# Kernel optimization log

Hardware: AMD Instinct MI355X
Metric: run time of the kernel (lower is better)

## Reference

```python
import jax, jax.numpy as jnp
import numpy as np
import math

D_MODEL = 1024
D_STATE = 16
D_CONV = 4
EXPAND = 2
D_INNER = EXPAND * D_MODEL
DT_RANK = max(D_MODEL // 16, 1)
B_SZ, L_SEQ = 2, 2048
DT_MIN, DT_MAX = 1e-3, 1e-1


def setup_inputs() -> dict:
    key = jax.random.key(0)
    ks = jax.random.split(key, 10)
    x = jax.random.normal(ks[0], (B_SZ, L_SEQ, D_MODEL), dtype=jnp.float32)
    # torch nn.Linear weights are [out, in]
    in_proj_w = jax.random.normal(ks[1], (2 * D_INNER, D_MODEL), jnp.float32) * 0.02
    conv_w = jax.random.normal(ks[2], (D_INNER, 1, D_CONV), jnp.float32) * 0.2  # depthwise [d,1,k]
    conv_b = jax.random.normal(ks[3], (D_INNER,), jnp.float32) * 0.02
    x_proj_w = jax.random.normal(ks[4], (DT_RANK + 2 * D_STATE, D_INNER), jnp.float32) * 0.02
    dt_init_std = DT_RANK ** -0.5
    dt_proj_w = jax.random.uniform(ks[5], (D_INNER, DT_RANK), jnp.float32, -dt_init_std, dt_init_std)
    dt = jnp.exp(jax.random.uniform(ks[6], (D_INNER,)) * (math.log(DT_MAX) - math.log(DT_MIN)) + math.log(DT_MIN))
    dt = jnp.clip(dt, DT_MIN, None)
    dt_proj_b = dt + jnp.log(-jnp.expm1(-dt))  # inverse softplus
    A = jnp.tile(jnp.arange(1, D_STATE + 1, dtype=jnp.float32)[None, :], (D_INNER, 1))
    A_log = jnp.log(A)
    D_param = jnp.ones((D_INNER,), jnp.float32)
    out_proj_w = jax.random.normal(ks[7], (D_MODEL, D_INNER), jnp.float32) * 0.02
    return {"x": x, "in_proj_w": in_proj_w, "conv_w": conv_w, "conv_b": conv_b,
            "x_proj_w": x_proj_w, "dt_proj_w": dt_proj_w, "dt_proj_b": dt_proj_b,
            "A_log": A_log, "D_param": D_param, "out_proj_w": out_proj_w}


def _ssm_forward(x, in_proj_w, conv_w, conv_b, x_proj_w, dt_proj_w, dt_proj_b, A_log, D_param, out_proj_w):
    B, L, _ = x.shape
    xz = jnp.einsum('bld,ed->ble', x, in_proj_w)          # [B,L,2*d_inner]
    x_branch, z = jnp.split(xz, 2, axis=-1)               # each [B,L,d_inner]
    # causal depthwise conv over L
    xc = jnp.transpose(x_branch, (0, 2, 1))               # [B,d,L]
    xc = jnp.pad(xc, ((0, 0), (0, 0), (D_CONV - 1, 0)))
    xc = jax.lax.conv_general_dilated(xc, conv_w, window_strides=(1,), padding='VALID',
                                      feature_group_count=D_INNER)
    xc = xc + conv_b[None, :, None]
    x_conv = jax.nn.silu(jnp.transpose(xc, (0, 2, 1)))    # [B,L,d_inner]
    # input-dependent projections
    xp = jnp.einsum('bld,ed->ble', x_conv, x_proj_w)      # [B,L,dt_rank+2n]
    dt_low, Bp, Cp = jnp.split(xp, [DT_RANK, DT_RANK + D_STATE], axis=-1)
    dt = jax.nn.softplus(jnp.einsum('blr,dr->bld', dt_low, dt_proj_w) + dt_proj_b)  # [B,L,d]
    A = -jnp.exp(A_log)                                   # [d,n]
    # sequential selective scan via lax.scan (time-major inputs)
    def step(h, inp):
        dt_t, B_t, C_t, x_t = inp                         # [B,d],[B,n],[B,n],[B,d]
        dA = jnp.exp(dt_t[:, :, None] * A[None])          # [B,d,n]
        h = dA * h + (dt_t * x_t)[:, :, None] * B_t[:, None, :]
        y = jnp.einsum('bdn,bn->bd', h, C_t)
        return h, y

    h0 = jnp.zeros((B, D_INNER, D_STATE), x.dtype)
    xs = (jnp.swapaxes(dt, 0, 1), jnp.swapaxes(Bp, 0, 1), jnp.swapaxes(Cp, 0, 1), jnp.swapaxes(x_conv, 0, 1))
    _, ys = jax.lax.scan(step, h0, xs)                    # ys: [L,B,d]
    y = jnp.swapaxes(ys, 0, 1)                            # [B,L,d]
    y = y + D_param * x_conv
    y = y * jax.nn.silu(z)
    return jnp.einsum('bld,ed->ble', y, out_proj_w)       # [B,L,d_model]


def reference(x, in_proj_w, conv_w, conv_b, x_proj_w, dt_proj_w, dt_proj_b, A_log, D_param, out_proj_w):
    return _ssm_forward(x, in_proj_w, conv_w, conv_b, x_proj_w, dt_proj_w, dt_proj_b, A_log, D_param, out_proj_w)
```

## Files before the change

### kernel.cpp

```cpp
#include <hip/hip_runtime.h>
#include <math.h>

#define BB      2
#define LSEQ    2048
#define DMODEL  1024
#define DINNER  2048
#define DSTATE  16
#define DTRANK  64
#define NPROJ   96
#define MROWS   (BB * LSEQ)
#define NCHUNK  64
#define CLEN    32
#define XKS     16

typedef short bf16x8 __attribute__((ext_vector_type(8)));
typedef float f32x4  __attribute__((ext_vector_type(4)));

struct HL { unsigned int hx, hy, lx, ly; };

__device__ __forceinline__ HL cvt4(float4 v) {
  unsigned int ux = __float_as_uint(v.x), uy = __float_as_uint(v.y);
  unsigned int uz = __float_as_uint(v.z), uw = __float_as_uint(v.w);
  unsigned int tx = ux & 0xFFFF0000u, ty = uy & 0xFFFF0000u;
  unsigned int tz = uz & 0xFFFF0000u, tw = uw & 0xFFFF0000u;
  HL r;
  r.hx = (tx >> 16) | ty;
  r.hy = (tz >> 16) | tw;
  float lx = v.x - __uint_as_float(tx);
  float ly = v.y - __uint_as_float(ty);
  float lz = v.z - __uint_as_float(tz);
  float lw = v.w - __uint_as_float(tw);
  unsigned int a = __float_as_uint(lx); a += 0x7FFFu + ((a >> 16) & 1u);
  unsigned int b = __float_as_uint(ly); b += 0x7FFFu + ((b >> 16) & 1u);
  unsigned int c = __float_as_uint(lz); c += 0x7FFFu + ((c >> 16) & 1u);
  unsigned int d = __float_as_uint(lw); d += 0x7FFFu + ((d >> 16) & 1u);
  r.lx = (a >> 16) | (b & 0xFFFF0000u);
  r.ly = (c >> 16) | (d & 0xFFFF0000u);
  return r;
}

__device__ __forceinline__ void stage2(unsigned short (*S)[128 * 32], int srow,
                                       int skf, const float4* va, const float4* vb) {
  const int sw = (srow >> 1) & 3;
  const int s0 = skf >> 3;
  const int o0 = srow * 32 + ((s0 ^ sw) << 3);
  const int o1 = srow * 32 + (((s0 + 1) ^ sw) << 3);
  HL a0 = cvt4(va[0]), a1 = cvt4(va[1]), a2 = cvt4(va[2]), a3 = cvt4(va[3]);
  *(uint4*)(S[0] + o0) = make_uint4(a0.hx, a0.hy, a1.hx, a1.hy);
  *(uint4*)(S[0] + o1) = make_uint4(a2.hx, a2.hy, a3.hx, a3.hy);
  *(uint4*)(S[1] + o0) = make_uint4(a0.lx, a0.ly, a1.lx, a1.ly);
  *(uint4*)(S[1] + o1) = make_uint4(a2.lx, a2.ly, a3.lx, a3.ly);
  HL b0 = cvt4(vb[0]), b1 = cvt4(vb[1]), b2 = cvt4(vb[2]), b3 = cvt4(vb[3]);
  *(uint4*)(S[2] + o0) = make_uint4(b0.hx, b0.hy, b1.hx, b1.hy);
  *(uint4*)(S[2] + o1) = make_uint4(b2.hx, b2.hy, b3.hx, b3.hy);
  *(uint4*)(S[3] + o0) = make_uint4(b0.lx, b0.ly, b1.lx, b1.ly);
  *(uint4*)(S[3] + o1) = make_uint4(b2.lx, b2.ly, b3.lx, b3.ly);
}

__global__ __launch_bounds__(256, 2)
void gemm_mfma(const float* __restrict__ A, const float* __restrict__ B,
               float* __restrict__ C0, float* __restrict__ C1,
               int M, int N, int K, int Nout) {
  __shared__ __align__(16) unsigned short SH[2][4][128 * 32];

  const int tid = threadIdx.x;
  const int nbx = N >> 7;
  const int qq  = gridDim.x >> 3;
  int flat = blockIdx.x;
  flat = (flat & 7) * qq + (flat >> 3);
  const int bx = flat % nbx, by = flat / nbx;
  const int row0 = by * 128, col0 = bx * 128;

  const int lane = tid & 63, wid = tid >> 6;
  const int wr = wid >> 1, wc = wid & 1;
  const int fr = lane & 15;
  const int g  = lane >> 4;

  const int srow = tid >> 1;
  const int skf  = (tid & 1) * 16;
  const float* aB = A + (size_t)(row0 + srow) * K + skf;
  const float* bB = B + (size_t)(col0 + srow) * K + skf;

  f32x4 acc[4][4] = {};
  const int NT = K >> 5;

  float4 cva[4], cvb[4];
#pragma unroll
  for (int q = 0; q < 4; ++q) {
    cva[q] = *(const float4*)(aB + q * 4);
    cvb[q] = *(const float4*)(bB + q * 4);
  }
  stage2(SH[0], srow, skf, cva, cvb);
#pragma unroll
  for (int q = 0; q < 4; ++q) {
    cva[q] = *(const float4*)(aB + 32 + q * 4);
    cvb[q] = *(const float4*)(bB + 32 + q * 4);
  }
  __syncthreads();

  int p = 0;
  for (int t = 0; t < NT; ++t) {
    bf16x8 bh[4], bl[4], ah[4], al[4];
#pragma unroll
    for (int j = 0; j < 4; ++j) {
      const int rb = wc * 64 + j * 16 + fr;
      const int ob = rb * 32 + (((g ^ (rb >> 1)) & 3) << 3);
      bh[j] = *(const bf16x8*)(SH[p][2] + ob);
      bl[j] = *(const bf16x8*)(SH[p][3] + ob);
    }
#pragma unroll
    for (int i = 0; i < 4; ++i) {
      const int ra = wr * 64 + i * 16 + fr;
      const int oa = ra * 32 + (((g ^ (ra >> 1)) & 3) << 3);
      ah[i] = *(const bf16x8*)(SH[p][0] + oa);
      al[i] = *(const bf16x8*)(SH[p][1] + oa);
    }
    if (t + 1 < NT) stage2(SH[p ^ 1], srow, skf, cva, cvb);
    if (t + 2 < NT) {
      const float* ap = aB + (size_t)(t + 2) * 32;
      const float* bp = bB + (size_t)(t + 2) * 32;
#pragma unroll
      for (int q = 0; q < 4; ++q) {
        cva[q] = *(const float4*)(ap + q * 4);
        cvb[q] = *(const float4*)(bp + q * 4);
      }
    }
#pragma unroll
    for (int i = 0; i < 4; ++i)
#pragma unroll
      for (int j = 0; j < 4; ++j) {
        acc[i][j] = __builtin_amdgcn_mfma_f32_16x16x32_bf16(al[i], bh[j], acc[i][j], 0, 0, 0);
        acc[i][j] = __builtin_amdgcn_mfma_f32_16x16x32_bf16(ah[i], bl[j], acc[i][j], 0, 0, 0);
        acc[i][j] = __builtin_amdgcn_mfma_f32_16x16x32_bf16(ah[i], bh[j], acc[i][j], 0, 0, 0);
      }
    __syncthreads();
    p ^= 1;
  }

  float* Cd;
  int cc0;
  if (C1 != nullptr && col0 >= Nout) { Cd = C1; cc0 = col0 - Nout; }
  else                               { Cd = C0; cc0 = col0; }
#pragma unroll
  for (int i = 0; i < 4; ++i) {
    const int rbase = row0 + wr * 64 + i * 16 + (lane >> 4) * 4;
#pragma unroll
    for (int j = 0; j < 4; ++j) {
      const int cc = cc0 + wc * 64 + j * 16 + fr;
#pragma unroll
      for (int r = 0; r < 4; ++r)
        Cd[(size_t)(rbase + r) * Nout + cc] = acc[i][j][r];
    }
  }
}

template <int ACT>
__global__ __launch_bounds__(256)
void gemm_tn(const float* __restrict__ A, const float* __restrict__ B,
             float* __restrict__ C, const float* __restrict__ bias,
             int M, int N, int K, int lda) {
  __shared__ float As[8][128];
  __shared__ float Bs[8][128];
  const int tid  = threadIdx.x;
  const int row0 = blockIdx.y * 128;
  const int col0 = blockIdx.x * 128;
  const int tx = tid & 15, ty = tid >> 4;
  const int lr = tid >> 1;
  const int lk = (tid & 1) * 4;

  float acc[8][8];
#pragma unroll
  for (int i = 0; i < 8; ++i)
#pragma unroll
    for (int j = 0; j < 8; ++j) acc[i][j] = 0.f;

  const float* Aptr = A + (size_t)(row0 + lr) * lda + lk;
  const int bcol = col0 + lr;
  const float* Bptr = (bcol < N) ? (B + (size_t)bcol * K + lk) : nullptr;

  float4 av = *(const float4*)(Aptr);
  float4 bv = Bptr ? *(const float4*)(Bptr) : make_float4(0.f, 0.f, 0.f, 0.f);

  for (int k0 = 0; k0 < K; k0 += 8) {
    As[lk + 0][lr] = av.x; As[lk + 1][lr] = av.y;
    As[lk + 2][lr] = av.z; As[lk + 3][lr] = av.w;
    Bs[lk + 0][lr] = bv.x; Bs[lk + 1][lr] = bv.y;
    Bs[lk + 2][lr] = bv.z; Bs[lk + 3][lr] = bv.w;
    if (k0 + 8 < K) {
      av = *(const float4*)(Aptr + k0 + 8);
      if (Bptr) bv = *(const float4*)(Bptr + k0 + 8);
    }
    __syncthreads();
#pragma unroll
    for (int k = 0; k < 8; ++k) {
      float a[8], b[8];
      *(float4*)&a[0] = *(const float4*)&As[k][ty * 4];
      *(float4*)&a[4] = *(const float4*)&As[k][64 + ty * 4];
      *(float4*)&b[0] = *(const float4*)&Bs[k][tx * 4];
      *(float4*)&b[4] = *(const float4*)&Bs[k][64 + tx * 4];
#pragma unroll
      for (int i = 0; i < 8; ++i)
#pragma unroll
        for (int j = 0; j < 8; ++j)
          acc[i][j] = fmaf(a[i], b[j], acc[i][j]);
    }
    __syncthreads();
  }

#pragma unroll
  for (int ih = 0; ih < 2; ++ih) {
#pragma unroll
    for (int i2 = 0; i2 < 4; ++i2) {
      int r = row0 + ih * 64 + ty * 4 + i2;
      if (r >= M) continue;
#pragma unroll
      for (int jh = 0; jh < 2; ++jh) {
        int c = col0 + jh * 64 + tx * 4;
        float vv[4];
#pragma unroll
        for (int j = 0; j < 4; ++j) {
          float v = acc[ih * 4 + i2][jh * 4 + j];
          if (ACT == 1) {
            v += bias[c + j];
            v = (v > 20.f) ? v : log1pf(expf(v));
          }
          vv[j] = v;
        }
        if (c + 3 < N) {
          *(float4*)(C + (size_t)r * N + c) = make_float4(vv[0], vv[1], vv[2], vv[3]);
        } else {
          for (int j = 0; j < 4; ++j)
            if (c + j < N) C[(size_t)r * N + c + j] = vv[j];
        }
      }
    }
  }
}

__global__ __launch_bounds__(256)
void xproj_splitk(const float* __restrict__ A, const float* __restrict__ W,
                  float* __restrict__ Pq) {
  __shared__ float As[8][128];
  __shared__ float Ws[8][96];
  const int tid  = threadIdx.x;
  const int row0 = blockIdx.x * 128;
  const int k0b  = blockIdx.y * (DINNER / XKS);
  const int tx = tid & 15, ty = tid >> 4;
  const int lr = tid >> 1, lk = (tid & 1) * 4;

  float acc[8][6];
#pragma unroll
  for (int i = 0; i < 8; ++i)
#pragma unroll
    for (int j = 0; j < 6; ++j) acc[i][j] = 0.f;

  const float* Ap = A + (size_t)(row0 + lr) * DINNER + lk;
  const float* Wp = (tid < 192) ? (W + (size_t)(tid >> 1) * DINNER + (tid & 1) * 4)
                                : nullptr;
  float4 av = *(const float4*)(Ap + k0b);
  float4 wv = Wp ? *(const float4*)(Wp + k0b) : make_float4(0.f, 0.f, 0.f, 0.f);

  for (int k0 = k0b; k0 < k0b + DINNER / XKS; k0 += 8) {
    As[lk + 0][lr] = av.x; As[lk + 1][lr] = av.y;
    As[lk + 2][lr] = av.z; As[lk + 3][lr] = av.w;
    if (Wp) {
      int j = tid >> 1, kk = (tid & 1) * 4;
      Ws[kk + 0][j] = wv.x; Ws[kk + 1][j] = wv.y;
      Ws[kk + 2][j] = wv.z; Ws[kk + 3][j] = wv.w;
    }
    if (k0 + 8 < k0b + DINNER / XKS) {
      av = *(const float4*)(Ap + k0 + 8);
      if (Wp) wv = *(const float4*)(Wp + k0 + 8);
    }
    __syncthreads();
#pragma unroll
    for (int kk = 0; kk < 8; ++kk) {
      float a[8], w[6];
      *(float4*)&a[0] = *(const float4*)&As[kk][ty * 8];
      *(float4*)&a[4] = *(const float4*)&As[kk][ty * 8 + 4];
#pragma unroll
      for (int j = 0; j < 6; ++j) w[j] = Ws[kk][tx * 6 + j];
#pragma unroll
      for (int i = 0; i < 8; ++i)
#pragma unroll
        for (int j = 0; j < 6; ++j)
          acc[i][j] = fmaf(a[i], w[j], acc[i][j]);
    }
    __syncthreads();
  }
  float* dst = Pq + (size_t)blockIdx.y * (MROWS * NPROJ);
#pragma unroll
  for (int i = 0; i < 8; ++i)
#pragma unroll
    for (int j = 0; j < 6; ++j)
      dst[(size_t)(row0 + ty * 8 + i) * NPROJ + tx * 6 + j] = acc[i][j];
}

__global__ __launch_bounds__(256)
void xpj_reduce(const float* __restrict__ Pq, float* __restrict__ xpb) {
  int idx = blockIdx.x * 256 + threadIdx.x;
  float s = 0.f;
#pragma unroll
  for (int q = 0; q < XKS; ++q)
    s += Pq[(size_t)q * (MROWS * NPROJ) + idx];
  xpb[idx] = s;
}

__global__ __launch_bounds__(256)
void conv_silu_kernel(const float* __restrict__ xb, const float* __restrict__ cw,
                      const float* __restrict__ cb, float* __restrict__ xc) {
  int idx = (blockIdx.x * 256 + threadIdx.x) * 4;
  int d  = idx & (DINNER - 1);
  int ml = idx >> 11;
  int l  = ml & (LSEQ - 1);
  float4 W0 = *(const float4*)(cw + (d + 0) * 4);
  float4 W1 = *(const float4*)(cw + (d + 1) * 4);
  float4 W2 = *(const float4*)(cw + (d + 2) * 4);
  float4 W3 = *(const float4*)(cw + (d + 3) * 4);
  const float* base = xb + (size_t)ml * DINNER + d;
  float4 z4 = make_float4(0.f, 0.f, 0.f, 0.f);
  float4 r0  = *(const float4*)(base);
  float4 rm1 = (l >= 1) ? *(const float4*)(base - DINNER)     : z4;
  float4 rm2 = (l >= 2) ? *(const float4*)(base - 2 * DINNER) : z4;
  float4 rm3 = (l >= 3) ? *(const float4*)(base - 3 * DINNER) : z4;
  float4 bias = *(const float4*)(cb + d);
  float4 o;
  o.x = bias.x + r0.x * W0.w + rm1.x * W0.z + rm2.x * W0.y + rm3.x * W0.x;
  o.y = bias.y + r0.y * W1.w + rm1.y * W1.z + rm2.y * W1.y + rm3.y * W1.x;
  o.z = bias.z + r0.z * W2.w + rm1.z * W2.z + rm2.z * W2.y + rm3.z * W2.x;
  o.w = bias.w + r0.w * W3.w + rm1.w * W3.z + rm2.w * W3.y + rm3.w * W3.x;
  o.x = o.x / (1.f + expf(-o.x));
  o.y = o.y / (1.f + expf(-o.y));
  o.z = o.z / (1.f + expf(-o.z));
  o.w = o.w / (1.f + expf(-o.w));
  *(float4*)(xc + idx) = o;
}

__global__ __launch_bounds__(256)
void scan_chunk_kernel(const float* __restrict__ dt, const float* __restrict__ xp,
                       const float* __restrict__ xc, const float* __restrict__ A_log,
                       float* __restrict__ P, float* __restrict__ H) {
  __shared__ float sbc[CLEN][32];
  const int tid = threadIdx.x;
  const int bid = blockIdx.x;
  const int b  = bid >> 9;
  const int c  = (bid >> 3) & 63;
  const int dg = bid & 7;
  const int d  = dg * 256 + tid;
  const int m0 = b * LSEQ + c * CLEN;
  {
    int r = tid >> 3, q = (tid & 7) * 4;
    *(float4*)&sbc[r][q] = *(const float4*)(xp + (size_t)(m0 + r) * NPROJ + DTRANK + q);
  }
  float a2[DSTATE], h[DSTATE];
#pragma unroll
  for (int n = 0; n < DSTATE; ++n) {
    a2[n] = -expf(A_log[d * DSTATE + n]) * 1.44269504f;
    h[n] = 0.f;
  }
  float dtsum = 0.f;
  __syncthreads();

  const float* dtp = dt + (size_t)m0 * DINNER + d;
  const float* xcp = xc + (size_t)m0 * DINNER + d;
  float ndt = dtp[0], nxc = xcp[0];
  for (int s = 0; s < CLEN; ++s) {
    float dtv = ndt, xv = nxc;
    int sp = (s + 1 < CLEN) ? s + 1 : s;
    ndt = dtp[(size_t)sp * DINNER];
    nxc = xcp[(size_t)sp * DINNER];
    dtsum += dtv;
    float dtx = dtv * xv;
    float Bv[16];
    *(float4*)&Bv[0]  = *(const float4*)&sbc[s][0];
    *(float4*)&Bv[4]  = *(const float4*)&sbc[s][4];
    *(float4*)&Bv[8]  = *(const float4*)&sbc[s][8];
    *(float4*)&Bv[12] = *(const float4*)&sbc[s][12];
#pragma unroll
    for (int n = 0; n < DSTATE; ++n) {
      float a = exp2f(dtv * a2[n]);
      h[n] = fmaf(a, h[n], dtx * Bv[n]);
    }
  }
  size_t o = ((size_t)(b * NCHUNK + c) * DINNER + d) * DSTATE;
  float4* Hp = (float4*)(H + o);
  Hp[0] = make_float4(h[0], h[1], h[2], h[3]);
  Hp[1] = make_float4(h[4], h[5], h[6], h[7]);
  Hp[2] = make_float4(h[8], h[9], h[10], h[11]);
  Hp[3] = make_float4(h[12], h[13], h[14], h[15]);
  float p[16];
#pragma unroll
  for (int n = 0; n < DSTATE; ++n) p[n] = exp2f(a2[n] * dtsum);
  float4* Pp = (float4*)(P + o);
  Pp[0] = make_float4(p[0], p[1], p[2], p[3]);
  Pp[1] = make_float4(p[4], p[5], p[6], p[7]);
  Pp[2] = make_float4(p[8], p[9], p[10], p[11]);
  Pp[3] = make_float4(p[12], p[13], p[14], p[15]);
}

__global__ __launch_bounds__(256)
void stitch_kernel(const float* __restrict__ P, float* __restrict__ H) {
  int idx = blockIdx.x * 256 + threadIdx.x;
  int b = idx >> 15, e = idx & 32767;
  size_t base = (size_t)b * NCHUNK * 32768 + e;
  float h = 0.f;
  for (int c = 0; c < NCHUNK; ++c) {
    size_t o = base + (size_t)c * 32768;
    float p = P[o], q = H[o];
    H[o] = h;
    h = fmaf(p, h, q);
  }
}

__global__ __launch_bounds__(256)
void scan_out_kernel(const float* dt, const float* __restrict__ xp,
                     const float* __restrict__ xc, const float* __restrict__ z,
                     const float* __restrict__ A_log, const float* __restrict__ Dp,
                     const float* __restrict__ Hinit, float* y) {
  __shared__ float sbc[CLEN][32];
  const int tid = threadIdx.x;
  const int bid = blockIdx.x;
  const int b  = bid >> 9;
  const int c  = (bid >> 3) & 63;
  const int dg = bid & 7;
  const int d  = dg * 256 + tid;
  const int m0 = b * LSEQ + c * CLEN;
  {
    int r = tid >> 3, q = (tid & 7) * 4;
    *(float4*)&sbc[r][q] = *(const float4*)(xp + (size_t)(m0 + r) * NPROJ + DTRANK + q);
  }
  float a2[DSTATE], h[DSTATE];
  size_t ho = ((size_t)(b * NCHUNK + c) * DINNER + d) * DSTATE;
  const float4* Hp = (const float4*)(Hinit + ho);
  float4 h0 = Hp[0], h1 = Hp[1], h2 = Hp[2], h3 = Hp[3];
  h[0]=h0.x; h[1]=h0.y; h[2]=h0.z; h[3]=h0.w;
  h[4]=h1.x; h[5]=h1.y; h[6]=h1.z; h[7]=h1.w;
  h[8]=h2.x; h[9]=h2.y; h[10]=h2.z; h[11]=h2.w;
  h[12]=h3.x; h[13]=h3.y; h[14]=h3.z; h[15]=h3.w;
#pragma unroll
  for (int n = 0; n < DSTATE; ++n)
    a2[n] = -expf(A_log[d * DSTATE + n]) * 1.44269504f;
  const float Dv = Dp[d];
  __syncthreads();

  const float* dtp = dt + (size_t)m0 * DINNER + d;
  const float* xcp = xc + (size_t)m0 * DINNER + d;
  const float* zp  = z  + (size_t)m0 * DINNER + d;
  float* yp = y + (size_t)m0 * DINNER + d;
  float ndt = dtp[0], nxc = xcp[0], nz = zp[0];
  for (int s = 0; s < CLEN; ++s) {
    float dtv = ndt, xv = nxc, zv = nz;
    int sp = (s + 1 < CLEN) ? s + 1 : s;
    ndt = dtp[(size_t)sp * DINNER];
    nxc = xcp[(size_t)sp * DINNER];
    nz  = zp[(size_t)sp * DINNER];
    float dtx = dtv * xv;
    float Bv[16], Cv[16];
    *(float4*)&Bv[0]  = *(const float4*)&sbc[s][0];
    *(float4*)&Bv[4]  = *(const float4*)&sbc[s][4];
    *(float4*)&Bv[8]  = *(const float4*)&sbc[s][8];
    *(float4*)&Bv[12] = *(const float4*)&sbc[s][12];
    *(float4*)&Cv[0]  = *(const float4*)&sbc[s][16];
    *(float4*)&Cv[4]  = *(const float4*)&sbc[s][20];
    *(float4*)&Cv[8]  = *(const float4*)&sbc[s][24];
    *(float4*)&Cv[12] = *(const float4*)&sbc[s][28];
    float yv = 0.f;
#pragma unroll
    for (int n = 0; n < DSTATE; ++n) {
      float a = exp2f(dtv * a2[n]);
      h[n] = fmaf(a, h[n], dtx * Bv[n]);
      yv = fmaf(h[n], Cv[n], yv);
    }
    yv = (yv + Dv * xv) * (zv / (1.f + expf(-zv)));
    yp[(size_t)s * DINNER] = yv;
  }
}

extern "C" void kernel_launch(void* const* d_in, const int* in_sizes, int n_in,
                              void* d_out, int out_size, void* d_ws, size_t ws_size,
                              hipStream_t stream) {
  const float* x          = (const float*)d_in[0];
  const float* in_proj_w  = (const float*)d_in[1];
  const float* conv_w     = (const float*)d_in[2];
  const float* conv_b     = (const float*)d_in[3];
  const float* x_proj_w   = (const float*)d_in[4];
  const float* dt_proj_w  = (const float*)d_in[5];
  const float* dt_proj_b  = (const float*)d_in[6];
  const float* A_log      = (const float*)d_in[7];
  const float* D_param    = (const float*)d_in[8];
  const float* out_proj_w = (const float*)d_in[9];
  float* out = (float*)d_out;
  float* ws  = (float*)d_ws;

  float* xb   = ws;
  float* dtr  = xb;
  float* zb   = ws + 8388608;
  float* xcb  = ws + 16777216;
  float* xpb  = ws + 25165824;
  float* Pbuf = ws + 25559040;
  float* Hbuf = ws + 29753344;
  float* Pq   = Pbuf;

  dim3 blk(256);
  gemm_mfma<<<dim3((MROWS / 128) * (2 * DINNER / 128)), blk, 0, stream>>>(
      x, in_proj_w, xb, zb, MROWS, 2 * DINNER, DMODEL, DINNER);
  conv_silu_kernel<<<(MROWS * DINNER) / 1024, blk, 0, stream>>>(xb, conv_w, conv_b, xcb);
  xproj_splitk<<<dim3(MROWS / 128, XKS), blk, 0, stream>>>(xcb, x_proj_w, Pq);
  xpj_reduce<<<(MROWS * NPROJ) / 256, blk, 0, stream>>>(Pq, xpb);
  gemm_tn<1><<<dim3(DINNER / 128, MROWS / 128), blk, 0, stream>>>(
      xpb, dt_proj_w, dtr, dt_proj_b, MROWS, DINNER, DTRANK, NPROJ);
  scan_chunk_kernel<<<dim3(BB * NCHUNK * 8), blk, 0, stream>>>(
      dtr, xpb, xcb, A_log, Pbuf, Hbuf);
  stitch_kernel<<<dim3(BB * DINNER * DSTATE / 256), blk, 0, stream>>>(Pbuf, Hbuf);
  scan_out_kernel<<<dim3(BB * NCHUNK * 8), blk, 0, stream>>>(
      dtr, xpb, xcb, zb, A_log, D_param, Hbuf, xb);
  gemm_mfma<<<dim3((MROWS / 128) * (DMODEL / 128)), blk, 0, stream>>>(
      xb, out_proj_w, out, out, MROWS, DMODEL, DINNER, DMODEL);
}
```

Measured before the change: 518.0 us.

## Pre-split GEMM operands into bf16 hi/lo buffers and load via global_load_lds

Adds a separate conversion kernel that splits fp32 activations and weights into bf16 high and low halves stored in workspace. The two MFMA GEMMs then copy these pre-split tiles straight from global memory into LDS with global_load_lds, replacing the in-kernel register staging and conversion. The register double-buffering is dropped in favour of a single LDS buffer with higher occupancy, and the tile-to-XCD mapping is changed. The cost is four extra conversion launches that read and write additional global memory on every call, and the loss of load/compute overlap inside each block.

After: 521.4 us. No clear change (+0.7%).

```diff
diff --git a/kernel.cpp b/kernel.cpp
--- a/kernel.cpp
+++ b/kernel.cpp
@@ -13,16 +13,17 @@
 #define CLEN    32
 #define XKS     16
 
+typedef unsigned short u16;
 typedef short bf16x8 __attribute__((ext_vector_type(8)));
 typedef float f32x4  __attribute__((ext_vector_type(4)));
 
 struct HL { unsigned int hx, hy, lx, ly; };
 
 __device__ __forceinline__ HL cvt4(float4 v) {
-  unsigned int ux = __float_as_uint(v.x), uy = __float_as_uint(v.y);
-  unsigned int uz = __float_as_uint(v.z), uw = __float_as_uint(v.w);
-  unsigned int tx = ux & 0xFFFF0000u, ty = uy & 0xFFFF0000u;
-  unsigned int tz = uz & 0xFFFF0000u, tw = uw & 0xFFFF0000u;
+  unsigned int tx = __float_as_uint(v.x) & 0xFFFF0000u;
+  unsigned int ty = __float_as_uint(v.y) & 0xFFFF0000u;
+  unsigned int tz = __float_as_uint(v.z) & 0xFFFF0000u;
+  unsigned int tw = __float_as_uint(v.w) & 0xFFFF0000u;
   HL r;
   r.hx = (tx >> 16) | ty;
   r.hy = (tz >> 16) | tw;
@@ -39,102 +40,85 @@
   return r;
 }
 
-__device__ __forceinline__ void stage2(unsigned short (*S)[128 * 32], int srow,
-                                       int skf, const float4* va, const float4* vb) {
-  const int sw = (srow >> 1) & 3;
-  const int s0 = skf >> 3;
-  const int o0 = srow * 32 + ((s0 ^ sw) << 3);
-  const int o1 = srow * 32 + (((s0 + 1) ^ sw) << 3);
-  HL a0 = cvt4(va[0]), a1 = cvt4(va[1]), a2 = cvt4(va[2]), a3 = cvt4(va[3]);
-  *(uint4*)(S[0] + o0) = make_uint4(a0.hx, a0.hy, a1.hx, a1.hy);
-  *(uint4*)(S[0] + o1) = make_uint4(a2.hx, a2.hy, a3.hx, a3.hy);
-  *(uint4*)(S[1] + o0) = make_uint4(a0.lx, a0.ly, a1.lx, a1.ly);
-  *(uint4*)(S[1] + o1) = make_uint4(a2.lx, a2.ly, a3.lx, a3.ly);
-  HL b0 = cvt4(vb[0]), b1 = cvt4(vb[1]), b2 = cvt4(vb[2]), b3 = cvt4(vb[3]);
-  *(uint4*)(S[2] + o0) = make_uint4(b0.hx, b0.hy, b1.hx, b1.hy);
-  *(uint4*)(S[2] + o1) = make_uint4(b2.hx, b2.hy, b3.hx, b3.hy);
-  *(uint4*)(S[3] + o0) = make_uint4(b0.lx, b0.ly, b1.lx, b1.ly);
-  *(uint4*)(S[3] + o1) = make_uint4(b2.lx, b2.ly, b3.lx, b3.ly);
-}
-
-__global__ __launch_bounds__(256, 2)
-void gemm_mfma(const float* __restrict__ A, const float* __restrict__ B,
-               float* __restrict__ C0, float* __restrict__ C1,
-               int M, int N, int K, int Nout) {
-  __shared__ __align__(16) unsigned short SH[2][4][128 * 32];
+__global__ __launch_bounds__(256)
+void cvt_hl(const float4* __restrict__ src, uint2* __restrict__ dh,
+            uint2* __restrict__ dl, int n4) {
+  int i = blockIdx.x * 256 + threadIdx.x;
+  if (i < n4) {
+    HL r = cvt4(src[i]);
+    dh[i] = make_uint2(r.hx, r.hy);
+    dl[i] = make_uint2(r.lx, r.ly);
+  }
+}
+
+__device__ __forceinline__ void gll16(const void* g, void* l) {
+  __builtin_amdgcn_global_load_lds(
+      (const __attribute__((address_space(1))) void*)g,
+      (__attribute__((address_space(3))) void*)l, 16, 0, 0);
+}
+
+__global__ __launch_bounds__(256, 3)
+void gemm_hl(const u16* __restrict__ Ahp, const u16* __restrict__ Alp,
+             const u16* __restrict__ Bhp, const u16* __restrict__ Blp,
+             float* __restrict__ C0, float* __restrict__ C1,
+             int M, int N, int K, int Nout, int XC_C) {
+  __shared__ __align__(16) u16 L[4][128 * 32];
 
   const int tid = threadIdx.x;
-  const int nbx = N >> 7;
-  const int qq  = gridDim.x >> 3;
-  int flat = blockIdx.x;
-  flat = (flat & 7) * qq + (flat >> 3);
-  const int bx = flat % nbx, by = flat / nbx;
-  const int row0 = by * 128, col0 = bx * 128;
-
-  const int lane = tid & 63, wid = tid >> 6;
-  const int wr = wid >> 1, wc = wid & 1;
-  const int fr = lane & 15;
-  const int g  = lane >> 4;
-
-  const int srow = tid >> 1;
-  const int skf  = (tid & 1) * 16;
-  const float* aB = A + (size_t)(row0 + srow) * K + skf;
-  const float* bB = B + (size_t)(col0 + srow) * K + skf;
+  const int nbx = N >> 7, nby = M >> 7;
+  const int xcd = blockIdx.x & 7;
+  const int pos = blockIdx.x >> 3;
+  const int cr = xcd / XC_C, cc = xcd - cr * XC_C;
+  const int GCc = nbx / XC_C;
+  const int GR  = (nby * XC_C) >> 3;
+  const int by = cr * GR + pos / GCc;
+  const int bx = cc * GCc + pos % GCc;
+  const int row0 = by << 7, col0 = bx << 7;
+
+  const int lane = tid & 63, w = tid >> 6;
+  const int wr = w >> 1, wc = w & 1;
+  const int fr = lane & 15, g = lane >> 4;
+  const int lrow = lane >> 2, lslot = lane & 3;
 
   f32x4 acc[4][4] = {};
-  const int NT = K >> 5;
-
-  float4 cva[4], cvb[4];
-#pragma unroll
-  for (int q = 0; q < 4; ++q) {
-    cva[q] = *(const float4*)(aB + q * 4);
-    cvb[q] = *(const float4*)(bB + q * 4);
-  }
-  stage2(SH[0], srow, skf, cva, cvb);
-#pragma unroll
-  for (int q = 0; q < 4; ++q) {
-    cva[q] = *(const float4*)(aB + 32 + q * 4);
-    cvb[q] = *(const float4*)(bB + 32 + q * 4);
-  }
-  __syncthreads();
-
-  int p = 0;
-  for (int t = 0; t < NT; ++t) {
-    bf16x8 bh[4], bl[4], ah[4], al[4];
+
+  for (int k0 = 0; k0 < K; k0 += 32) {
+#pragma unroll
+    for (int s = 0; s < 2; ++s) {
+      const int r = w * 32 + s * 16 + lrow;
+      const int csrc = (lslot ^ ((r >> 1) & 3)) << 3;
+      const size_t gA = (size_t)(row0 + r) * K + k0 + csrc;
+      const size_t gB = (size_t)(col0 + r) * K + k0 + csrc;
+      const int lb = w * 1024 + s * 512;
+      gll16(Ahp + gA, &L[0][lb]);
+      gll16(Alp + gA, &L[1][lb]);
+      gll16(Bhp + gB, &L[2][lb]);
+      gll16(Blp + gB, &L[3][lb]);
+    }
+    __syncthreads();
+
+    bf16x8 bh[4], bl[4];
 #pragma unroll
     for (int j = 0; j < 4; ++j) {
       const int rb = wc * 64 + j * 16 + fr;
-      const int ob = rb * 32 + (((g ^ (rb >> 1)) & 3) << 3);
-      bh[j] = *(const bf16x8*)(SH[p][2] + ob);
-      bl[j] = *(const bf16x8*)(SH[p][3] + ob);
+      const int o = rb * 32 + ((g ^ ((rb >> 1) & 3)) << 3);
+      bh[j] = *(const bf16x8*)&L[2][o];
+      bl[j] = *(const bf16x8*)&L[3][o];
     }
 #pragma unroll
     for (int i = 0; i < 4; ++i) {
       const int ra = wr * 64 + i * 16 + fr;
-      const int oa = ra * 32 + (((g ^ (ra >> 1)) & 3) << 3);
-      ah[i] = *(const bf16x8*)(SH[p][0] + oa);
-      al[i] = *(const bf16x8*)(SH[p][1] + oa);
-    }
-    if (t + 1 < NT) stage2(SH[p ^ 1], srow, skf, cva, cvb);
-    if (t + 2 < NT) {
-      const float* ap = aB + (size_t)(t + 2) * 32;
-      const float* bp = bB + (size_t)(t + 2) * 32;
-#pragma unroll
-      for (int q = 0; q < 4; ++q) {
-        cva[q] = *(const float4*)(ap + q * 4);
-        cvb[q] = *(const float4*)(bp + q * 4);
+      const int o = ra * 32 + ((g ^ ((ra >> 1) & 3)) << 3);
+      bf16x8 ah = *(const bf16x8*)&L[0][o];
+      bf16x8 al = *(const bf16x8*)&L[1][o];
+#pragma unroll
+      for (int j = 0; j < 4; ++j) {
+        acc[i][j] = __builtin_amdgcn_mfma_f32_16x16x32_bf16(al, bh[j], acc[i][j], 0, 0, 0);
+        acc[i][j] = __builtin_amdgcn_mfma_f32_16x16x32_bf16(ah, bl[j], acc[i][j], 0, 0, 0);
+        acc[i][j] = __builtin_amdgcn_mfma_f32_16x16x32_bf16(ah, bh[j], acc[i][j], 0, 0, 0);
       }
     }
-#pragma unroll
-    for (int i = 0; i < 4; ++i)
-#pragma unroll
-      for (int j = 0; j < 4; ++j) {
-        acc[i][j] = __builtin_amdgcn_mfma_f32_16x16x32_bf16(al[i], bh[j], acc[i][j], 0, 0, 0);
-        acc[i][j] = __builtin_amdgcn_mfma_f32_16x16x32_bf16(ah[i], bl[j], acc[i][j], 0, 0, 0);
-        acc[i][j] = __builtin_amdgcn_mfma_f32_16x16x32_bf16(ah[i], bh[j], acc[i][j], 0, 0, 0);
-      }
     __syncthreads();
-    p ^= 1;
   }
 
   float* Cd;
@@ -146,10 +130,10 @@
     const int rbase = row0 + wr * 64 + i * 16 + (lane >> 4) * 4;
 #pragma unroll
     for (int j = 0; j < 4; ++j) {
-      const int cc = cc0 + wc * 64 + j * 16 + fr;
+      const int cfull = cc0 + wc * 64 + j * 16 + fr;
 #pragma unroll
       for (int r = 0; r < 4; ++r)
-        Cd[(size_t)(rbase + r) * Nout + cc] = acc[i][j][r];
+        Cd[(size_t)(rbase + r) * Nout + cfull] = acc[i][j][r];
     }
   }
 }
@@ -501,9 +485,20 @@
   float* Hbuf = ws + 29753344;
   float* Pq   = Pbuf;
 
+  u16* xh = (u16*)(ws + 16777216);
+  u16* xl = (u16*)(ws + 16777216 + 2097152);
+  u16* wh = (u16*)(ws + 16777216 + 4194304);
+  u16* wl = (u16*)(ws + 16777216 + 6291456);
+  u16* yh = (u16*)(ws + 16777216);
+  u16* yl = (u16*)(ws + 16777216 + 4194304);
+  u16* oh = (u16*)(ws + 25559040);
+  u16* ol = (u16*)(ws + 25559040 + 1048576);
+
   dim3 blk(256);
-  gemm_mfma<<<dim3((MROWS / 128) * (2 * DINNER / 128)), blk, 0, stream>>>(
-      x, in_proj_w, xb, zb, MROWS, 2 * DINNER, DMODEL, DINNER);
+  cvt_hl<<<4096, blk, 0, stream>>>((const float4*)x, (uint2*)xh, (uint2*)xl, 1048576);
+  cvt_hl<<<4096, blk, 0, stream>>>((const float4*)in_proj_w, (uint2*)wh, (uint2*)wl, 1048576);
+  gemm_hl<<<dim3((MROWS / 128) * (2 * DINNER / 128)), blk, 0, stream>>>(
+      xh, xl, wh, wl, xb, zb, MROWS, 2 * DINNER, DMODEL, DINNER, 4);
   conv_silu_kernel<<<(MROWS * DINNER) / 1024, blk, 0, stream>>>(xb, conv_w, conv_b, xcb);
   xproj_splitk<<<dim3(MROWS / 128, XKS), blk, 0, stream>>>(xcb, x_proj_w, Pq);
   xpj_reduce<<<(MROWS * NPROJ) / 256, blk, 0, stream>>>(Pq, xpb);
@@ -514,6 +509,8 @@
   stitch_kernel<<<dim3(BB * DINNER * DSTATE / 256), blk, 0, stream>>>(Pbuf, Hbuf);
   scan_out_kernel<<<dim3(BB * NCHUNK * 8), blk, 0, stream>>>(
       dtr, xpb, xcb, zb, A_log, D_param, Hbuf, xb);
-  gemm_mfma<<<dim3((MROWS / 128) * (DMODEL / 128)), blk, 0, stream>>>(
-      xb, out_proj_w, out, out, MROWS, DMODEL, DINNER, DMODEL);
-}
+  cvt_hl<<<8192, blk, 0, stream>>>((const float4*)xb, (uint2*)yh, (uint2*)yl, 2097152);
+  cvt_hl<<<2048, blk, 0, stream>>>((const float4*)out_proj_w, (uint2*)oh, (uint2*)ol, 524288);
+  gemm_hl<<<dim3((MROWS / 128) * (DMODEL / 128)), blk, 0, stream>>>(
+      yh, yl, oh, ol, out, out, MROWS, DMODEL, DINNER, DMODEL, 1);
+}
```
